# Performance work log

Measured on AMD Instinct MI355X. Metric: run time of the kernel, lower is better.

The kernel has to match this reference:

```python
import jax, jax.numpy as jnp
import numpy as np

E = 8      # num experts
K = 2      # top-k
D = 1024   # hidden size
F = 4096   # intermediate size
B, S = 4, 1024


def setup_inputs() -> dict:
    key = jax.random.key(0)
    ks = jax.random.split(key, 5)
    s = 0.02
    return {
        "hidden_states": jax.random.normal(ks[0], (B, S, D), jnp.float32),
        "gate_w": jax.random.normal(ks[1], (D, E), jnp.float32) * s,   # Linear, no bias
        "fc_w": jax.random.normal(ks[2], (E, D, F), jnp.float32) * s,  # Conv1D weight [in,out]
        "fc_b": jnp.zeros((E, F), jnp.float32),
        "proj_w": jax.random.normal(ks[3], (E, F, D), jnp.float32) * s,
        "proj_b": jnp.zeros((E, D), jnp.float32),
    }


def reference(hidden_states, gate_w, fc_w, fc_b, proj_w, proj_b):
    b, s, d = hidden_states.shape
    x = hidden_states.reshape(-1, d)                       # [T, D]
    router_logits = x @ gate_w                             # [T, E]
    probs = jax.nn.softmax(router_logits.astype(jnp.float32), axis=-1)
    routing_weights, selected_experts = jax.lax.top_k(probs, K)   # [T, K]
    routing_weights = routing_weights / routing_weights.sum(-1, keepdims=True)
    routing_weights = routing_weights.astype(x.dtype)

    out = jnp.zeros_like(x)
    # Fixed small loop over experts (structurally distinct weights).
    # Dense mask-weighted compute == gather/MLP/scatter-add of the original
    # (tokens not routed to expert e get weight 0).
    for e in range(E):
        w_e = jnp.sum(routing_weights * (selected_experts == e), axis=-1)  # [T]
        h = jax.nn.gelu(x @ fc_w[e] + fc_b[e], approximate=True)           # gelu_new
        h = h @ proj_w[e] + proj_b[e]
        out = out + h * w_e[:, None]

    return out.reshape(b, s, d), router_logits
```

## Files before the change

kernel.cpp:

```cpp
#include <hip/hip_runtime.h>
#include <hip/hip_bf16.h>


#define T_TOK 4096
#define D_DIM 1024
#define F_DIM 4096
#define E_NUM 8
#define CAP   9216

typedef short short8 __attribute__((ext_vector_type(8)));
typedef float f32x4  __attribute__((ext_vector_type(4)));

__device__ __forceinline__ void async_ld16(const void* g, void* l) {
  __builtin_amdgcn_global_load_lds(
      (const __attribute__((address_space(1))) char*)g,
      (__attribute__((address_space(3))) char*)l,
      16, 0, 0);
}

__global__ void transpose_cast(const float* __restrict__ in, __hip_bfloat16* __restrict__ out,
                               int R, int C) {
  __shared__ float tile[32][33];
  const int ex = blockIdx.z;
  const float* inp = in + (size_t)ex * R * C;
  __hip_bfloat16* outp = out + (size_t)ex * R * C;
  const int c0 = blockIdx.x * 32, r0 = blockIdx.y * 32;
  const int tx = threadIdx.x & 31, ty = threadIdx.x >> 5;
#pragma unroll
  for (int i = 0; i < 4; ++i)
    tile[ty + i * 8][tx] = inp[(size_t)(r0 + ty + i * 8) * C + c0 + tx];
  __syncthreads();
#pragma unroll
  for (int i = 0; i < 4; ++i)
    outp[(size_t)(c0 + ty + i * 8) * R + r0 + tx] = __float2bfloat16(tile[tx][ty + i * 8]);
}

__global__ void router_kernel(const float* __restrict__ x, const float* __restrict__ gw,
                              float* __restrict__ logits, int* __restrict__ counts,
                              int* __restrict__ tk_e, int* __restrict__ tk_pos,
                              float* __restrict__ tk_w) {
  const int lane = threadIdx.x & 63;
  const int t = blockIdx.x * 4 + (threadIdx.x >> 6);
  const float* xr = x + (size_t)t * D_DIM;
  float a[8] = {0.f, 0.f, 0.f, 0.f, 0.f, 0.f, 0.f, 0.f};
  for (int it = 0; it < D_DIM / 64; ++it) {
    const int d = lane + it * 64;
    const float xv = xr[d];
    const float4 g0 = *(const float4*)(gw + d * 8);
    const float4 g1 = *(const float4*)(gw + d * 8 + 4);
    a[0] += xv * g0.x; a[1] += xv * g0.y; a[2] += xv * g0.z; a[3] += xv * g0.w;
    a[4] += xv * g1.x; a[5] += xv * g1.y; a[6] += xv * g1.z; a[7] += xv * g1.w;
  }
#pragma unroll
  for (int off = 32; off > 0; off >>= 1)
#pragma unroll
    for (int e = 0; e < 8; ++e) a[e] += __shfl_down(a[e], off);
  if (lane == 0) {
    float mx = a[0];
#pragma unroll
    for (int e = 1; e < 8; ++e) mx = fmaxf(mx, a[e]);
    float p[8], s = 0.f;
#pragma unroll
    for (int e = 0; e < 8; ++e) { p[e] = expf(a[e] - mx); s += p[e]; }
    (void)s;
    int i1 = 0;
#pragma unroll
    for (int e = 1; e < 8; ++e) if (p[e] > p[i1]) i1 = e;
    int i2 = (i1 == 0) ? 1 : 0;
#pragma unroll
    for (int e = 0; e < 8; ++e) if (e != i1 && p[e] > p[i2]) i2 = e;
    const float inv = 1.f / (p[i1] + p[i2]);
#pragma unroll
    for (int e = 0; e < 8; ++e) logits[(size_t)t * 8 + e] = a[e];
    const int p1 = atomicAdd(counts + i1, 1);
    const int p2 = atomicAdd(counts + i2, 1);
    tk_e[t * 2]     = i1; tk_pos[t * 2]     = p1; tk_w[t * 2]     = p[i1] * inv;
    tk_e[t * 2 + 1] = i2; tk_pos[t * 2 + 1] = p2; tk_w[t * 2 + 1] = p[i2] * inv;
  }
}

__global__ void prefix_kernel(const int* __restrict__ counts, int* __restrict__ bases) {
  if (threadIdx.x == 0 && blockIdx.x == 0) {
    int b = 0;
    for (int e = 0; e < 8; ++e) { bases[e] = b; b += (counts[e] + 127) & ~127; }
    bases[8] = b;
  }
}

__global__ void gather_kernel(const float* __restrict__ x, const int* __restrict__ bases,
                              const int* __restrict__ tk_e, const int* __restrict__ tk_pos,
                              const float* __restrict__ tk_w,
                              __hip_bfloat16* __restrict__ Xg,
                              int* __restrict__ slot_token, float* __restrict__ slot_weight) {
  const int b = blockIdx.x;
  const int t = b >> 1;
  const int slot = bases[tk_e[b]] + tk_pos[b];
  if (threadIdx.x == 0) { slot_token[slot] = t; slot_weight[slot] = tk_w[b]; }
  const float4 v = ((const float4*)(x + (size_t)t * D_DIM))[threadIdx.x];
  union { __hip_bfloat16 h[4]; ushort4 u; } pk;
  pk.h[0] = __float2bfloat16(v.x);
  pk.h[1] = __float2bfloat16(v.y);
  pk.h[2] = __float2bfloat16(v.z);
  pk.h[3] = __float2bfloat16(v.w);
  ((ushort4*)(Xg + (size_t)slot * D_DIM))[threadIdx.x] = pk.u;
}

template <int N, int K, bool IS_FC>
__global__ __launch_bounds__(256, 2) void moe_gemm(
    const __hip_bfloat16* __restrict__ A, const __hip_bfloat16* __restrict__ Bt,
    const float* __restrict__ bias, const int* __restrict__ counts,
    const int* __restrict__ bases, __hip_bfloat16* __restrict__ Hout,
    const int* __restrict__ slot_token, const float* __restrict__ slot_weight,
    float* __restrict__ out) {
  __shared__ __align__(16) __hip_bfloat16 As[128 * 32];
  __shared__ __align__(16) __hip_bfloat16 Bs[128 * 32];

  const int m0 = blockIdx.y * 128;
  const int total = bases[8];
  if (m0 >= total) return;
  int e = 0;
#pragma unroll
  for (int i = 1; i < 8; ++i) e = (m0 >= bases[i]) ? i : e;
  const int n0 = blockIdx.x * 128;

  const __hip_bfloat16* Ab = A + (size_t)m0 * K;
  const __hip_bfloat16* Bb = Bt + ((size_t)e * N + n0) * K;

  const int tid = threadIdx.x;
  const int lane = tid & 63;
  const int wave = tid >> 6;
  const int wm = (wave >> 1) * 64;
  const int wn = (wave & 1) * 64;
  const int lr = lane & 15;
  const int quad = lane >> 4;

  f32x4 acc[4][4] = {};

  const int c0 = tid, c1 = tid + 256;
  const int ar0 = c0 >> 2, ac0 = (c0 & 3) * 8;
  const int ar1 = c1 >> 2, ac1 = (c1 & 3) * 8;

  for (int k0 = 0; k0 < K; k0 += 32) {
    async_ld16(Ab + (size_t)ar0 * K + k0 + ac0, As + c0 * 8);
    async_ld16(Ab + (size_t)ar1 * K + k0 + ac1, As + c1 * 8);
    async_ld16(Bb + (size_t)ar0 * K + k0 + ac0, Bs + c0 * 8);
    async_ld16(Bb + (size_t)ar1 * K + k0 + ac1, Bs + c1 * 8);
    __syncthreads();

    short8 af[4], bfr[4];
#pragma unroll
    for (int i = 0; i < 4; ++i)
      af[i] = *(const short8*)(As + (wm + i * 16 + lr) * 32 + quad * 8);
#pragma unroll
    for (int j = 0; j < 4; ++j)
      bfr[j] = *(const short8*)(Bs + (wn + j * 16 + lr) * 32 + quad * 8);
#pragma unroll
    for (int i = 0; i < 4; ++i)
#pragma unroll
      for (int j = 0; j < 4; ++j)
        acc[i][j] = __builtin_amdgcn_mfma_f32_16x16x32_bf16(af[i], bfr[j], acc[i][j], 0, 0, 0);
    __syncthreads();
  }

  if (IS_FC) {
#pragma unroll
    for (int j = 0; j < 4; ++j) {
      const int nc = n0 + wn + j * 16 + lr;
      const float bv = bias[(size_t)e * N + nc];
#pragma unroll
      for (int i = 0; i < 4; ++i) {
#pragma unroll
        for (int r = 0; r < 4; ++r) {
          const int row = m0 + wm + i * 16 + quad * 4 + r;
          float v = acc[i][j][r] + bv;
          float u = v + 0.044715f * v * v * v;
          float g = 0.5f * v * (1.0f + tanhf(0.79788456080286536f * u));
          Hout[(size_t)row * N + nc] = __float2bfloat16(g);
        }
      }
    }
  } else {
    const int base_e = bases[e];
    const int cnt = counts[e];
#pragma unroll
    for (int i = 0; i < 4; ++i) {
#pragma unroll
      for (int r = 0; r < 4; ++r) {
        const int row = m0 + wm + i * 16 + quad * 4 + r;
        if (row - base_e < cnt) {
          const float w = slot_weight[row];
          const int t = slot_token[row];
          float* orow = out + (size_t)t * D_DIM;
#pragma unroll
          for (int j = 0; j < 4; ++j) {
            const int nc = n0 + wn + j * 16 + lr;
            atomicAdd(orow + nc, (acc[i][j][r] + bias[(size_t)e * N + nc]) * w);
          }
        }
      }
    }
  }
}

extern "C" void kernel_launch(void* const* d_in, const int* in_sizes, int n_in,
                              void* d_out, int out_size, void* d_ws, size_t ws_size,
                              hipStream_t stream) {
  const float* x      = (const float*)d_in[0];
  const float* gate_w = (const float*)d_in[1];
  const float* fc_w   = (const float*)d_in[2];
  const float* fc_b   = (const float*)d_in[3];
  const float* proj_w = (const float*)d_in[4];
  const float* proj_b = (const float*)d_in[5];
  float* out = (float*)d_out;
  float* logits = out + (size_t)T_TOK * D_DIM;

  char* ws = (char*)d_ws;
  __hip_bfloat16* fcT   = (__hip_bfloat16*)(ws);
  __hip_bfloat16* projT = (__hip_bfloat16*)(ws + 67108864LL);
  __hip_bfloat16* Xg    = (__hip_bfloat16*)(ws + 134217728LL);
  __hip_bfloat16* Hg    = (__hip_bfloat16*)(ws + 153092096LL);
  int* meta = (int*)(ws + 228589568LL);
  int*   counts      = meta;
  int*   bases       = meta + 8;
  int*   tk_e        = meta + 20;
  int*   tk_pos      = tk_e + 8192;
  float* tk_w        = (float*)(tk_pos + 8192);
  int*   slot_token  = (int*)(tk_w + 8192);
  float* slot_weight = (float*)(slot_token + CAP);

  hipMemsetAsync(d_out, 0, (size_t)out_size * sizeof(float), stream);
  hipMemsetAsync(counts, 0, 8 * sizeof(int), stream);

  transpose_cast<<<dim3(F_DIM / 32, D_DIM / 32, E_NUM), 256, 0, stream>>>(fc_w, fcT, D_DIM, F_DIM);
  transpose_cast<<<dim3(D_DIM / 32, F_DIM / 32, E_NUM), 256, 0, stream>>>(proj_w, projT, F_DIM, D_DIM);

  router_kernel<<<T_TOK / 4, 256, 0, stream>>>(x, gate_w, logits, counts, tk_e, tk_pos, tk_w);
  prefix_kernel<<<1, 64, 0, stream>>>(counts, bases);
  gather_kernel<<<T_TOK * 2, 256, 0, stream>>>(x, bases, tk_e, tk_pos, tk_w, Xg,
                                               slot_token, slot_weight);

  moe_gemm<F_DIM, D_DIM, true><<<dim3(F_DIM / 128, CAP / 128), 256, 0, stream>>>(
      Xg, fcT, fc_b, counts, bases, Hg, nullptr, nullptr, nullptr);
  moe_gemm<D_DIM, F_DIM, false><<<dim3(D_DIM / 128, CAP / 128), 256, 0, stream>>>(
      Hg, projT, proj_b, counts, bases, nullptr, slot_token, slot_weight, out);
}
```

Baseline: 716.8 us.

## Split-K the proj GEMM, vectorize weight transpose, and use fast exp GELU

The proj GEMM now splits its K=4096 reduction across four blocks along grid z. The partial sums are combined through the existing atomicAdd epilogue, and only the z=0 slice adds the bias. The goal is more blocks for a grid that was only 8 columns wide, paid for with four times as many output atomics. The weight transpose now uses 64x64 tiles with float4 loads and 8-byte bf16 stores. GELU's tanh is rewritten as v*sigmoid(2u) using __expf, and the router softmax also switches to __expf.

```diff
diff --git a/kernel.cpp b/kernel.cpp
--- a/kernel.cpp
+++ b/kernel.cpp
@@ -20,19 +20,29 @@
 
 __global__ void transpose_cast(const float* __restrict__ in, __hip_bfloat16* __restrict__ out,
                                int R, int C) {
-  __shared__ float tile[32][33];
+  __shared__ float t[64][65];
   const int ex = blockIdx.z;
-  const float* inp = in + (size_t)ex * R * C;
-  __hip_bfloat16* outp = out + (size_t)ex * R * C;
-  const int c0 = blockIdx.x * 32, r0 = blockIdx.y * 32;
-  const int tx = threadIdx.x & 31, ty = threadIdx.x >> 5;
-#pragma unroll
-  for (int i = 0; i < 4; ++i)
-    tile[ty + i * 8][tx] = inp[(size_t)(r0 + ty + i * 8) * C + c0 + tx];
+  in  += (size_t)ex * R * C;
+  out += (size_t)ex * R * C;
+  const int r0 = blockIdx.y * 64, c0 = blockIdx.x * 64;
+  const int tx = threadIdx.x & 15;
+  const int ty = threadIdx.x >> 4;
+#pragma unroll
+  for (int i = 0; i < 4; ++i) {
+    const int r = ty + i * 16;
+    const float4 v = *(const float4*)(in + (size_t)(r0 + r) * C + c0 + tx * 4);
+    t[r][tx * 4 + 0] = v.x; t[r][tx * 4 + 1] = v.y;
+    t[r][tx * 4 + 2] = v.z; t[r][tx * 4 + 3] = v.w;
+  }
   __syncthreads();
 #pragma unroll
-  for (int i = 0; i < 4; ++i)
-    outp[(size_t)(c0 + ty + i * 8) * R + r0 + tx] = __float2bfloat16(tile[tx][ty + i * 8]);
+  for (int i = 0; i < 4; ++i) {
+    const int c = ty + i * 16;
+    union { __hip_bfloat16 h[4]; ushort4 u; } pk;
+#pragma unroll
+    for (int k = 0; k < 4; ++k) pk.h[k] = __float2bfloat16(t[tx * 4 + k][c]);
+    *(ushort4*)(out + (size_t)(c0 + c) * R + r0 + tx * 4) = pk.u;
+  }
 }
 
 __global__ void router_kernel(const float* __restrict__ x, const float* __restrict__ gw,
@@ -59,10 +69,9 @@
     float mx = a[0];
 #pragma unroll
     for (int e = 1; e < 8; ++e) mx = fmaxf(mx, a[e]);
-    float p[8], s = 0.f;
-#pragma unroll
-    for (int e = 0; e < 8; ++e) { p[e] = expf(a[e] - mx); s += p[e]; }
-    (void)s;
+    float p[8];
+#pragma unroll
+    for (int e = 0; e < 8; ++e) p[e] = __expf(a[e] - mx);
     int i1 = 0;
 #pragma unroll
     for (int e = 1; e < 8; ++e) if (p[e] > p[i1]) i1 = e;
@@ -105,7 +114,7 @@
   ((ushort4*)(Xg + (size_t)slot * D_DIM))[threadIdx.x] = pk.u;
 }
 
-template <int N, int K, bool IS_FC>
+template <int N, int K, int KSPLIT, bool IS_FC>
 __global__ __launch_bounds__(256, 2) void moe_gemm(
     const __hip_bfloat16* __restrict__ A, const __hip_bfloat16* __restrict__ Bt,
     const float* __restrict__ bias, const int* __restrict__ counts,
@@ -122,9 +131,11 @@
 #pragma unroll
   for (int i = 1; i < 8; ++i) e = (m0 >= bases[i]) ? i : e;
   const int n0 = blockIdx.x * 128;
-
-  const __hip_bfloat16* Ab = A + (size_t)m0 * K;
-  const __hip_bfloat16* Bb = Bt + ((size_t)e * N + n0) * K;
+  constexpr int KC = K / KSPLIT;
+  const int kbase = blockIdx.z * KC;
+
+  const __hip_bfloat16* Ab = A + (size_t)m0 * K + kbase;
+  const __hip_bfloat16* Bb = Bt + ((size_t)e * N + n0) * K + kbase;
 
   const int tid = threadIdx.x;
   const int lane = tid & 63;
@@ -140,7 +151,7 @@
   const int ar0 = c0 >> 2, ac0 = (c0 & 3) * 8;
   const int ar1 = c1 >> 2, ac1 = (c1 & 3) * 8;
 
-  for (int k0 = 0; k0 < K; k0 += 32) {
+  for (int k0 = 0; k0 < KC; k0 += 32) {
     async_ld16(Ab + (size_t)ar0 * K + k0 + ac0, As + c0 * 8);
     async_ld16(Ab + (size_t)ar1 * K + k0 + ac1, As + c1 * 8);
     async_ld16(Bb + (size_t)ar0 * K + k0 + ac0, Bs + c0 * 8);
@@ -172,9 +183,9 @@
 #pragma unroll
         for (int r = 0; r < 4; ++r) {
           const int row = m0 + wm + i * 16 + quad * 4 + r;
-          float v = acc[i][j][r] + bv;
-          float u = v + 0.044715f * v * v * v;
-          float g = 0.5f * v * (1.0f + tanhf(0.79788456080286536f * u));
+          const float v = acc[i][j][r] + bv;
+          const float u2 = 1.5957691216057308f * (v + 0.044715f * v * v * v);
+          const float g = v / (1.0f + __expf(-u2));
           Hout[(size_t)row * N + nc] = __float2bfloat16(g);
         }
       }
@@ -182,6 +193,7 @@
   } else {
     const int base_e = bases[e];
     const int cnt = counts[e];
+    const float bscale = (blockIdx.z == 0) ? 1.0f : 0.0f;
 #pragma unroll
     for (int i = 0; i < 4; ++i) {
 #pragma unroll
@@ -194,7 +206,7 @@
 #pragma unroll
           for (int j = 0; j < 4; ++j) {
             const int nc = n0 + wn + j * 16 + lr;
-            atomicAdd(orow + nc, (acc[i][j][r] + bias[(size_t)e * N + nc]) * w);
+            atomicAdd(orow + nc, (acc[i][j][r] + bscale * bias[(size_t)e * N + nc]) * w);
           }
         }
       }
@@ -231,16 +243,16 @@
   hipMemsetAsync(d_out, 0, (size_t)out_size * sizeof(float), stream);
   hipMemsetAsync(counts, 0, 8 * sizeof(int), stream);
 
-  transpose_cast<<<dim3(F_DIM / 32, D_DIM / 32, E_NUM), 256, 0, stream>>>(fc_w, fcT, D_DIM, F_DIM);
-  transpose_cast<<<dim3(D_DIM / 32, F_DIM / 32, E_NUM), 256, 0, stream>>>(proj_w, projT, F_DIM, D_DIM);
+  transpose_cast<<<dim3(F_DIM / 64, D_DIM / 64, E_NUM), 256, 0, stream>>>(fc_w, fcT, D_DIM, F_DIM);
+  transpose_cast<<<dim3(D_DIM / 64, F_DIM / 64, E_NUM), 256, 0, stream>>>(proj_w, projT, F_DIM, D_DIM);
 
   router_kernel<<<T_TOK / 4, 256, 0, stream>>>(x, gate_w, logits, counts, tk_e, tk_pos, tk_w);
   prefix_kernel<<<1, 64, 0, stream>>>(counts, bases);
   gather_kernel<<<T_TOK * 2, 256, 0, stream>>>(x, bases, tk_e, tk_pos, tk_w, Xg,
                                                slot_token, slot_weight);
 
-  moe_gemm<F_DIM, D_DIM, true><<<dim3(F_DIM / 128, CAP / 128), 256, 0, stream>>>(
+  moe_gemm<F_DIM, D_DIM, 1, true><<<dim3(F_DIM / 128, CAP / 128, 1), 256, 0, stream>>>(
       Xg, fcT, fc_b, counts, bases, Hg, nullptr, nullptr, nullptr);
-  moe_gemm<D_DIM, F_DIM, false><<<dim3(D_DIM / 128, CAP / 128), 256, 0, stream>>>(
+  moe_gemm<D_DIM, F_DIM, 4, false><<<dim3(D_DIM / 128, CAP / 128, 4), 256, 0, stream>>>(
       Hg, projT, proj_b, counts, bases, nullptr, slot_token, slot_weight, out);
 }
```

New measurement: 757.4 us. +5.7%, slower.
